# Performance work log

Measured on AMD Instinct MI355X. Metric: run time of the kernel, lower is better.

The kernel has to match this reference:

```python
import jax, jax.numpy as jnp
import numpy as np

D_MODEL = 1024
N_HEADS = 16
HEAD_DIM = D_MODEL // N_HEADS  # 64
WINDOW = 15
NUM_RANDOM = 2
B, L = 2, 2048


def setup_inputs() -> dict:
    key = jax.random.key(0)
    ks = jax.random.split(key, 5)
    x = jax.random.normal(ks[0], (B, L, D_MODEL), dtype=jnp.float32)
    # rotary angles: theta[t, j] = t / 10000^(2j/head_dim), shape [1, L, head_dim//2]
    inv_freq = 1.0 / (10000.0 ** (jnp.arange(0, HEAD_DIM, 2, dtype=jnp.float32) / HEAD_DIM))
    t = jnp.arange(L, dtype=jnp.float32)
    freqs = (t[:, None] * inv_freq[None, :])[None].astype(jnp.float32)  # [1,L,32]
    scale = 0.02
    wq = jax.random.normal(ks[1], (D_MODEL, D_MODEL), dtype=jnp.float32) * scale
    wk = jax.random.normal(ks[2], (D_MODEL, D_MODEL), dtype=jnp.float32) * scale
    wv = jax.random.normal(ks[3], (D_MODEL, D_MODEL), dtype=jnp.float32) * scale
    wo = jax.random.normal(ks[4], (D_MODEL, D_MODEL), dtype=jnp.float32) * scale
    return {"x": x, "freqs": freqs, "wq": wq, "wk": wk, "wv": wv, "wo": wo}


def _rope(t, cos, sin):
    # t: [B,H,L,hd]; interpret last dim as (hd/2, 2) complex pairs and rotate.
    tr = t.reshape(*t.shape[:-1], -1, 2)
    re, im = tr[..., 0], tr[..., 1]
    out_re = re * cos - im * sin
    out_im = re * sin + im * cos
    return jnp.stack([out_re, out_im], axis=-1).reshape(t.shape)


def _bigbird_mask(Lq):
    ii = jnp.arange(Lq)[:, None]
    jj = jnp.arange(Lq)[None, :]
    causal = jj <= ii
    window = jnp.abs(ii - jj) <= (WINDOW // 2)
    glob = (ii == 0) | (jj == 0)
    # random mask: per row i, NUM_RANDOM indices uniform in [0, i]
    rkey = jax.random.key(42)
    u = jax.random.uniform(rkey, (Lq, NUM_RANDOM))
    ridx = jnp.floor(u * (jnp.arange(Lq, dtype=jnp.float32)[:, None] + 1.0)).astype(jnp.int32)
    rmask = jnp.zeros((Lq, Lq), dtype=bool).at[jnp.arange(Lq)[:, None], ridx].set(True)
    # rows with <= NUM_RANDOM causal options attend to all of them
    rmask = rmask | (causal & (ii < NUM_RANDOM))
    return (causal & (window | rmask)) | glob  # [L,L]


def reference(x, freqs, wq, wk, wv, wo):
    b, l, _ = x.shape
    q = (x @ wq.T).reshape(b, l, N_HEADS, HEAD_DIM).transpose(0, 2, 1, 3)  # [B,H,L,hd]
    k = (x @ wk.T).reshape(b, l, N_HEADS, HEAD_DIM).transpose(0, 2, 1, 3)
    v = (x @ wv.T).reshape(b, l, N_HEADS, HEAD_DIM).transpose(0, 2, 1, 3)
    cos = jnp.cos(freqs[:, :l])[:, None]  # [1,1,L,hd/2]
    sin = jnp.sin(freqs[:, :l])[:, None]
    q = _rope(q, cos, sin)
    k = _rope(k, cos, sin)
    attn_mask = _bigbird_mask(l)  # [L,L], broadcast over B,H
    scale = 1.0 / jnp.sqrt(jnp.float32(HEAD_DIM))
    scores = jnp.einsum("bhqd,bhkd->bhqk", q, k) * scale
    scores = jnp.where(attn_mask[None, None], scores, jnp.finfo(scores.dtype).min)
    p = jax.nn.softmax(scores, axis=-1)
    out = jnp.einsum("bhqk,bhkd->bhqd", p, v)
    out = out.transpose(0, 2, 1, 3).reshape(b, l, D_MODEL)
    return out @ wo.T
```

## Files before the change

### kernel.cpp

```cpp
#include <hip/hip_runtime.h>
#include <math.h>

#define SEQ_L 2048
#define DM 1024
#define NH 16
#define HD 64
#define NB 2
#define KD 1024
#define ND 1024

typedef __bf16 bf16;
typedef __bf16 bf16x8 __attribute__((ext_vector_type(8)));
typedef __bf16 bf16x4 __attribute__((ext_vector_type(4)));
typedef __bf16 bf16x2 __attribute__((ext_vector_type(2)));
typedef float f32x4 __attribute__((ext_vector_type(4)));

__device__ inline uint32_t rotl32(uint32_t v, int n) { return (v << n) | (v >> (32 - n)); }

__device__ inline void threefry(uint32_t x0, uint32_t x1, uint32_t* o0, uint32_t* o1) {
  const uint32_t ks0 = 0u, ks1 = 42u, ks2 = 0u ^ 42u ^ 0x1BD11BDAu;
  x0 += ks0; x1 += ks1;
#define TF_R(rr) { x0 += x1; x1 = rotl32(x1, rr); x1 ^= x0; }
  TF_R(13) TF_R(15) TF_R(26) TF_R(6)
  x0 += ks1; x1 += ks2 + 1u;
  TF_R(17) TF_R(29) TF_R(16) TF_R(24)
  x0 += ks2; x1 += ks0 + 2u;
  TF_R(13) TF_R(15) TF_R(26) TF_R(6)
  x0 += ks0; x1 += ks1 + 3u;
  TF_R(17) TF_R(29) TF_R(16) TF_R(24)
  x0 += ks1; x1 += ks2 + 4u;
  TF_R(13) TF_R(15) TF_R(26) TF_R(6)
  x0 += ks2; x1 += ks0 + 5u;
#undef TF_R
  *o0 = x0; *o1 = x1;
}

__device__ inline int rand_col(int i, int s) {
  uint32_t o0, o1;
  threefry(0u, (uint32_t)(2 * i + s), &o0, &o1);
  uint32_t bits = o0 ^ o1;
  float u = __uint_as_float((bits >> 9) | 0x3f800000u) - 1.0f;
  return (int)floorf(u * (float)(i + 1));
}

__global__ void prep_kernel(const float* __restrict__ x,
                            const float* __restrict__ w0, const float* __restrict__ w1,
                            const float* __restrict__ w2, const float* __restrict__ w3,
                            const float* __restrict__ freqs,
                            bf16* __restrict__ xb,
                            bf16* __restrict__ o0, bf16* __restrict__ o1,
                            bf16* __restrict__ o2, bf16* __restrict__ o3,
                            int* __restrict__ ctab, float2* __restrict__ rtab) {
  const int bx = blockIdx.x;
  const int t = threadIdx.x;
  if (bx < 8192) {
    const float* src;
    bf16* dst;
    int idx;
    if (bx < 4096) { src = x; dst = xb; idx = bx * 256 + t; }
    else {
      int widx = bx - 4096;
      int wsel = widx >> 10;
      switch (wsel) {
        case 0: src = w0; dst = o0; break;
        case 1: src = w1; dst = o1; break;
        case 2: src = w2; dst = o2; break;
        default: src = w3; dst = o3; break;
      }
      idx = (widx & 1023) * 256 + t;
    }
    float4 vv = ((const float4*)src)[idx];
    bf16x4 ov;
    ov[0] = (bf16)vv.x; ov[1] = (bf16)vv.y; ov[2] = (bf16)vv.z; ov[3] = (bf16)vv.w;
    *(bf16x4*)(dst + (size_t)idx * 4) = ov;
    return;
  }
  if (bx < 8200) {
    const int i = (bx - 8192) * 256 + t;
    int cols[11]; int nc = 0;
    if (i >= 1) {
      int lo = i - 7; if (lo < 0) lo = 0;
      for (int j = lo; j <= i; ++j) cols[nc++] = j;
      if (lo > 0) cols[nc++] = 0;
#pragma unroll
      for (int s = 0; s < 2; ++s) {
        int rj = rand_col(i, s);
        bool dup = false;
        for (int c2 = 0; c2 < nc; ++c2) dup |= (cols[c2] == rj);
        if (!dup) cols[nc++] = rj;
      }
    }
    for (int c2 = nc; c2 < 11; ++c2) cols[c2] = -1;
#pragma unroll
    for (int c2 = 0; c2 < 11; ++c2) ctab[i * 12 + c2] = cols[c2];
    ctab[i * 12 + 11] = nc;
    return;
  }
  const int idx = (bx - 8200) * 256 + t;
  float s, c;
  sincosf(freqs[idx], &s, &c);
  rtab[idx] = make_float2(c, s);
}

__device__ inline void gld16(const bf16* g, bf16* l) {
  __builtin_amdgcn_global_load_lds((const __attribute__((address_space(1))) void*)g,
                                   (__attribute__((address_space(3))) void*)l, 16, 0, 0);
}

__global__ __launch_bounds__(256, 4) void qkv_gemm_kernel(
    const bf16* __restrict__ xb, const bf16* __restrict__ wqb, const bf16* __restrict__ wkb,
    const bf16* __restrict__ wvb, bf16* __restrict__ qb, bf16* __restrict__ kb, bf16* __restrict__ vb,
    const float2* __restrict__ rtab) {
  __shared__ __align__(16) bf16 As[64 * 64];
  __shared__ __align__(16) bf16 Bs[3][64 * 64];
  const bf16* Ws[3] = {wqb, wkb, wvb};
  bf16* Ds[3] = {qb, kb, vb};

  const int t = threadIdx.x;
  const int lane = t & 63;
  const int w = t >> 6;
  const int wm = (w >> 1) * 32;
  const int wn = (w & 1) * 32;
  const int m0 = blockIdx.x * 64;
  const int n0 = blockIdx.y * 64;
  const int l15 = lane & 15;
  const int kq = lane >> 4;

  f32x4 acc[3][2][2] = {};

  for (int k0 = 0; k0 < KD; k0 += 64) {
#pragma unroll
    for (int n = 0; n < 2; ++n) {
      const int s = n * 256 + t;
      const int row = s >> 3;
      const int ch = (s & 7) ^ (row & 7);
      gld16(xb + (size_t)(m0 + row) * KD + k0 + ch * 8, As + s * 8);
    }
#pragma unroll
    for (int j = 0; j < 3; ++j)
#pragma unroll
      for (int n = 0; n < 2; ++n) {
        const int s = n * 256 + t;
        const int row = s >> 3;
        const int ch = (s & 7) ^ (row & 7);
        gld16(Ws[j] + (size_t)(n0 + row) * KD + k0 + ch * 8, &Bs[j][s * 8]);
      }
    __syncthreads();
#pragma unroll
    for (int ks = 0; ks < 2; ++ks) {
      const int cb = ks * 4 + kq;
      bf16x8 af[2];
#pragma unroll
      for (int mt = 0; mt < 2; ++mt) {
        const int row = wm + mt * 16 + l15;
        af[mt] = *(const bf16x8*)(As + row * 64 + ((cb ^ (row & 7)) * 8));
      }
#pragma unroll
      for (int j = 0; j < 3; ++j) {
        bf16x8 bfr[2];
#pragma unroll
        for (int nt = 0; nt < 2; ++nt) {
          const int row = wn + nt * 16 + l15;
          bfr[nt] = *(const bf16x8*)(&Bs[j][row * 64 + ((cb ^ (row & 7)) * 8)]);
        }
#pragma unroll
        for (int mt = 0; mt < 2; ++mt)
#pragma unroll
          for (int nt = 0; nt < 2; ++nt)
            acc[j][mt][nt] = __builtin_amdgcn_mfma_f32_16x16x32_bf16(af[mt], bfr[nt], acc[j][mt][nt], 0, 0, 0);
      }
    }
    __syncthreads();
  }
  const int colb = n0 + wn + l15;
  const int rowb = m0 + wm + (lane >> 4) * 4;
  const int odd = l15 & 1;
#pragma unroll
  for (int j = 0; j < 3; ++j) {
    bf16* D = Ds[j];
    const bool dorope = (j < 2);
#pragma unroll
    for (int mt = 0; mt < 2; ++mt)
#pragma unroll
      for (int nt = 0; nt < 2; ++nt) {
        const int col = colb + nt * 16;
        const int jj = (col & 63) >> 1;
#pragma unroll
        for (int rr = 0; rr < 4; ++rr) {
          float val = acc[j][mt][nt][rr];
          float other = __shfl_xor(val, 1);
          if (!odd) {
            const int row = rowb + mt * 16 + rr;
            float lo, hi;
            if (dorope) {
              float2 cs = rtab[(row & (SEQ_L - 1)) * 32 + jj];
              lo = val * cs.x - other * cs.y;
              hi = val * cs.y + other * cs.x;
            } else { lo = val; hi = other; }
            bf16x2 p; p[0] = (bf16)lo; p[1] = (bf16)hi;
            *(bf16x2*)(D + (size_t)row * ND + col) = p;
          }
        }
      }
  }
}

__global__ __launch_bounds__(256, 2) void out_gemm_kernel(
    bf16* __restrict__ ab, const bf16* __restrict__ wob, float* __restrict__ out,
    const float* __restrict__ pm, const float* __restrict__ pz, const float* __restrict__ pv) {
  const int t = threadIdx.x;
  const int m0 = blockIdx.x * 64;
  const int n0 = blockIdx.y * 128;

  if (blockIdx.x == 0 || blockIdx.x == 32) {
    const int b = blockIdx.x == 0 ? 0 : 1;
#pragma unroll
    for (int e = t; e < DM; e += 256) {
      const int h = e >> 6, d = e & 63;
      const int base = b * 128 + h * 8;
      float M = -1e30f;
#pragma unroll
      for (int c = 0; c < 8; ++c) M = fmaxf(M, pm[base + c]);
      float Z = 0.f, od = 0.f;
#pragma unroll
      for (int c = 0; c < 8; ++c) {
        float sc = __expf(pm[base + c] - M);
        Z += pz[base + c] * sc;
        od += pv[(base + c) * 64 + d] * sc;
      }
      ab[(size_t)b * SEQ_L * DM + e] = (bf16)(od / Z);
    }
    __syncthreads();
  }

  __shared__ __align__(16) bf16 As[64 * 64];
  __shared__ __align__(16) bf16 Bs[128 * 64];
  const int lane = t & 63;
  const int wave = t >> 6;
  const int wm = (wave >> 1) * 32;
  const int wn = (wave & 1) * 64;
  const int l15 = lane & 15;
  const int kq = lane >> 4;

  f32x4 acc[2][4] = {};

  for (int k0 = 0; k0 < KD; k0 += 64) {
#pragma unroll
    for (int n = 0; n < 2; ++n) {
      const int s = n * 256 + t;
      const int row = s >> 3;
      const int ch = (s & 7) ^ (row & 7);
      gld16(ab + (size_t)(m0 + row) * KD + k0 + ch * 8, As + s * 8);
    }
#pragma unroll
    for (int n = 0; n < 4; ++n) {
      const int s = n * 256 + t;
      const int row = s >> 3;
      const int ch = (s & 7) ^ (row & 7);
      gld16(wob + (size_t)(n0 + row) * KD + k0 + ch * 8, Bs + s * 8);
    }
    __syncthreads();
#pragma unroll
    for (int ks = 0; ks < 2; ++ks) {
      const int cb = ks * 4 + kq;
      bf16x8 af[2], bfr[4];
#pragma unroll
      for (int mt = 0; mt < 2; ++mt) {
        const int row = wm + mt * 16 + l15;
        af[mt] = *(const bf16x8*)(As + row * 64 + ((cb ^ (row & 7)) * 8));
      }
#pragma unroll
      for (int nt = 0; nt < 4; ++nt) {
        const int row = wn + nt * 16 + l15;
        bfr[nt] = *(const bf16x8*)(Bs + row * 64 + ((cb ^ (row & 7)) * 8));
      }
#pragma unroll
      for (int mt = 0; mt < 2; ++mt)
#pragma unroll
        for (int nt = 0; nt < 4; ++nt)
          acc[mt][nt] = __builtin_amdgcn_mfma_f32_16x16x32_bf16(af[mt], bfr[nt], acc[mt][nt], 0, 0, 0);
    }
    __syncthreads();
  }
  const int colb = n0 + wn + l15;
  const int rowb = m0 + wm + (lane >> 4) * 4;
#pragma unroll
  for (int mt = 0; mt < 2; ++mt)
#pragma unroll
    for (int nt = 0; nt < 4; ++nt)
#pragma unroll
      for (int rr = 0; rr < 4; ++rr)
        out[(size_t)(rowb + mt * 16 + rr) * ND + colb + nt * 16] = acc[mt][nt][rr];
}

__global__ __launch_bounds__(256, 3) void attn_kernel(const bf16* __restrict__ q, const bf16* __restrict__ k,
                                                      const bf16* __restrict__ v, bf16* __restrict__ o,
                                                      const int* __restrict__ ctab,
                                                      float* __restrict__ pm, float* __restrict__ pz,
                                                      float* __restrict__ pv) {
  const int t = threadIdx.x;
  const int lane = t & 63;
  const int w = t >> 6;

  __shared__ float sbuf[256];
  __shared__ float redm[4], redz[4];
  __shared__ float part[4][64];

  if (blockIdx.x >= 256) {
    const int sbx = blockIdx.x - 256;
    const int b = sbx >> 9;
    const int tt = sbx & 511;
    const int tile = ((tt & 7) << 6) + (tt >> 3);
    const int i = tile * 4 + 1 + w;
    if (i >= SEQ_L) return;
    const size_t bb = (size_t)b * SEQ_L * DM;
    const int eo = lane * 16;

    const bf16* qrow = q + bb + (size_t)i * DM + eo;
    bf16x8 qv0 = *(const bf16x8*)(qrow);
    bf16x8 qv1 = *(const bf16x8*)(qrow + 8);

    const int4* cp = (const int4*)(ctab + i * 12);
    int4 ca = cp[0], cb = cp[1], cc = cp[2];
    int cols[11] = {ca.x, ca.y, ca.z, ca.w, cb.x, cb.y, cb.z, cb.w, cc.x, cc.y, cc.z};

    bf16x8 kv[11][2];
#pragma unroll
    for (int c = 0; c < 11; ++c) {
      int cj = cols[c] < 0 ? 0 : cols[c];
      const bf16* krow = k + bb + (size_t)cj * DM + eo;
      kv[c][0] = *(const bf16x8*)(krow);
      kv[c][1] = *(const bf16x8*)(krow + 8);
    }

    float sv[11];
#pragma unroll
    for (int c = 0; c < 11; ++c) {
      float acc = 0.f;
#pragma unroll
      for (int e = 0; e < 8; ++e)
        acc += (float)qv0[e] * (float)kv[c][0][e] + (float)qv1[e] * (float)kv[c][1][e];
      sv[c] = acc;
    }

    bf16x8 vv[11][2];
#pragma unroll
    for (int c = 0; c < 11; ++c) {
      int cj = cols[c] < 0 ? 0 : cols[c];
      const bf16* vrow = v + bb + (size_t)cj * DM + eo;
      vv[c][0] = *(const bf16x8*)(vrow);
      vv[c][1] = *(const bf16x8*)(vrow + 8);
    }

#pragma unroll
    for (int c = 0; c < 11; ++c) {
      sv[c] += __shfl_xor(sv[c], 1);
      sv[c] += __shfl_xor(sv[c], 2);
      sv[c] = cols[c] < 0 ? -1e30f : sv[c] * 0.125f;
    }
    float m = -1e30f;
#pragma unroll
    for (int c = 0; c < 11; ++c) m = fmaxf(m, sv[c]);
    float z = 0.f;
#pragma unroll
    for (int c = 0; c < 11; ++c) { sv[c] = __expf(sv[c] - m); z += sv[c]; }
    const float inv = 1.f / z;

    float oa[16] = {};
#pragma unroll
    for (int c = 0; c < 11; ++c) {
#pragma unroll
      for (int e = 0; e < 8; ++e) {
        oa[e]     += sv[c] * (float)vv[c][0][e];
        oa[8 + e] += sv[c] * (float)vv[c][1][e];
      }
    }
    bf16x8 ov0, ov1;
#pragma unroll
    for (int e = 0; e < 8; ++e) {
      ov0[e] = (bf16)(oa[e] * inv);
      ov1[e] = (bf16)(oa[8 + e] * inv);
    }
    bf16* orow = o + bb + (size_t)i * DM + eo;
    *(bf16x8*)(orow) = ov0;
    *(bf16x8*)(orow + 8) = ov1;
    return;
  }

  const int idx = blockIdx.x;
  const int b = idx >> 7;
  const int rem = idx & 127;
  const int h = rem >> 3;
  const int c = rem & 7;
  const size_t hb = (size_t)b * SEQ_L * DM + (size_t)h * HD;
  const int j = c * 256 + t;

  bf16x8 qv8[8];
#pragma unroll
  for (int cc = 0; cc < 8; ++cc) qv8[cc] = *(const bf16x8*)(q + hb + cc * 8);

  float acc = 0.f;
#pragma unroll
  for (int cc = 0; cc < 8; ++cc) {
    bf16x8 kv = *(const bf16x8*)(k + hb + (size_t)j * DM + cc * 8);
#pragma unroll
    for (int e = 0; e < 8; ++e) acc += (float)qv8[cc][e] * (float)kv[e];
  }
  float s = acc * 0.125f;
  float mloc = s;
#pragma unroll
  for (int off = 32; off > 0; off >>= 1) mloc = fmaxf(mloc, __shfl_xor(mloc, off));
  if (lane == 0) redm[w] = mloc;
  __syncthreads();
  const float m = fmaxf(fmaxf(redm[0], redm[1]), fmaxf(redm[2], redm[3]));

  float e = __expf(s - m);
  sbuf[t] = e;
  float zloc = e;
#pragma unroll
  for (int off = 32; off > 0; off >>= 1) zloc += __shfl_xor(zloc, off);
  if (lane == 0) redz[w] = zloc;
  __syncthreads();
  const float zc = redz[0] + redz[1] + redz[2] + redz[3];

  float oa = 0.f;
  for (int jj = w; jj < 256; jj += 4)
    oa += sbuf[jj] * (float)v[hb + (size_t)(c * 256 + jj) * DM + lane];
  part[w][lane] = oa;
  __syncthreads();
  if (t < 64) pv[idx * 64 + t] = part[0][t] + part[1][t] + part[2][t] + part[3][t];
  if (t == 0) { pm[idx] = m; pz[idx] = zc; }
}

extern "C" void kernel_launch(void* const* d_in, const int* in_sizes, int n_in,
                              void* d_out, int out_size, void* d_ws, size_t ws_size,
                              hipStream_t stream) {
  const float* x     = (const float*)d_in[0];
  const float* freqs = (const float*)d_in[1];
  const float* wq    = (const float*)d_in[2];
  const float* wk    = (const float*)d_in[3];
  const float* wv    = (const float*)d_in[4];
  const float* wo    = (const float*)d_in[5];
  float* out = (float*)d_out;

  char* ws = (char*)d_ws;
  bf16* xb  = (bf16*)(ws + 0);
  bf16* wqb = (bf16*)(ws + 8388608);
  bf16* wkb = (bf16*)(ws + 10485760);
  bf16* wvb = (bf16*)(ws + 12582912);
  bf16* wob = (bf16*)(ws + 14680064);
  bf16* qb  = (bf16*)(ws + 16777216);
  bf16* kb  = (bf16*)(ws + 25165824);
  bf16* vb  = (bf16*)(ws + 33554432);
  bf16* ab  = (bf16*)(ws + 41943040);
  int*    ctab = (int*)(ws + 50331648);
  float*  pm   = (float*)(ws + 50462720);
  float*  pz   = (float*)(ws + 50463744);
  float*  pv   = (float*)(ws + 50464768);
  float2* rtab = (float2*)(ws + 50593792);
  (void)ws_size;

  prep_kernel<<<8456, 256, 0, stream>>>(x, wq, wk, wv, wo, freqs, xb, wqb, wkb, wvb, wob, ctab, rtab);
  qkv_gemm_kernel<<<dim3(64, 16), 256, 0, stream>>>(xb, wqb, wkb, wvb, qb, kb, vb, rtab);
  attn_kernel<<<dim3(1280, 1), 256, 0, stream>>>(qb, kb, vb, ab, ctab, pm, pz, pv);
  out_gemm_kernel<<<dim3(64, 8), 256, 0, stream>>>(ab, wob, out, pm, pz, pv);
}
```

Before: 161.1 us.

## Double-buffer LDS tiles with BK=32 in QKV and output GEMMs

Both GEMM kernels (the fused QKV projection with RoPE and the output projection) now use two LDS buffers with a K-tile of 32 instead of a single 64-wide tile. The next tile's global-to-LDS loads are issued before computing on the current tile, so load latency overlaps with MFMA work. The XOR swizzle is adapted to the 32-wide rows and pointer offsets are precomputed. The trade-off is twice as many barriers per K, and each inner step does less MFMA work, which gives less to hide latency behind. The total LDS footprint is unchanged.

Result: slower. 169.6 us (+5.3%).

```diff
diff --git a/kernel.cpp b/kernel.cpp
--- a/kernel.cpp
+++ b/kernel.cpp
@@ -111,9 +111,8 @@
     const bf16* __restrict__ xb, const bf16* __restrict__ wqb, const bf16* __restrict__ wkb,
     const bf16* __restrict__ wvb, bf16* __restrict__ qb, bf16* __restrict__ kb, bf16* __restrict__ vb,
     const float2* __restrict__ rtab) {
-  __shared__ __align__(16) bf16 As[64 * 64];
-  __shared__ __align__(16) bf16 Bs[3][64 * 64];
-  const bf16* Ws[3] = {wqb, wkb, wvb};
+  __shared__ __align__(16) bf16 As0[64 * 32], As1[64 * 32];
+  __shared__ __align__(16) bf16 Bs0[3][64 * 32], Bs1[3][64 * 32];
   bf16* Ds[3] = {qb, kb, vb};
 
   const int t = threadIdx.x;
@@ -126,52 +125,60 @@
   const int l15 = lane & 15;
   const int kq = lane >> 4;
 
+  const int r0 = t >> 2;
+  const int chs = (t & 3) ^ ((r0 >> 1) & 3);
+  const size_t soff = (size_t)r0 * KD + chs * 8;
+  const bf16* pA  = xb  + (size_t)m0 * KD + soff;
+  const bf16* pB0 = wqb + (size_t)n0 * KD + soff;
+  const bf16* pB1 = wkb + (size_t)n0 * KD + soff;
+  const bf16* pB2 = wvb + (size_t)n0 * KD + soff;
+  const int t8 = t * 8;
+
   f32x4 acc[3][2][2] = {};
 
-  for (int k0 = 0; k0 < KD; k0 += 64) {
-#pragma unroll
-    for (int n = 0; n < 2; ++n) {
-      const int s = n * 256 + t;
-      const int row = s >> 3;
-      const int ch = (s & 7) ^ (row & 7);
-      gld16(xb + (size_t)(m0 + row) * KD + k0 + ch * 8, As + s * 8);
-    }
-#pragma unroll
-    for (int j = 0; j < 3; ++j)
-#pragma unroll
-      for (int n = 0; n < 2; ++n) {
-        const int s = n * 256 + t;
-        const int row = s >> 3;
-        const int ch = (s & 7) ^ (row & 7);
-        gld16(Ws[j] + (size_t)(n0 + row) * KD + k0 + ch * 8, &Bs[j][s * 8]);
-      }
+  auto stage = [&](int kt, bf16* A, bf16* B0, bf16* B1, bf16* B2) {
+    const int koff = kt * 32;
+    gld16(pA + koff, A + t8);
+    gld16(pB0 + koff, B0 + t8);
+    gld16(pB1 + koff, B1 + t8);
+    gld16(pB2 + koff, B2 + t8);
+  };
+  auto comp = [&](const bf16* A, const bf16* B0, const bf16* B1, const bf16* B2) {
+    bf16x8 af[2];
+#pragma unroll
+    for (int mt = 0; mt < 2; ++mt) {
+      const int row = wm + mt * 16 + l15;
+      af[mt] = *(const bf16x8*)(A + row * 32 + ((kq ^ ((row >> 1) & 3)) * 8));
+    }
+    const bf16* Bp[3] = {B0, B1, B2};
+#pragma unroll
+    for (int j = 0; j < 3; ++j) {
+      bf16x8 bfr[2];
+#pragma unroll
+      for (int nt = 0; nt < 2; ++nt) {
+        const int row = wn + nt * 16 + l15;
+        bfr[nt] = *(const bf16x8*)(Bp[j] + row * 32 + ((kq ^ ((row >> 1) & 3)) * 8));
+      }
+#pragma unroll
+      for (int mt = 0; mt < 2; ++mt)
+#pragma unroll
+        for (int nt = 0; nt < 2; ++nt)
+          acc[j][mt][nt] = __builtin_amdgcn_mfma_f32_16x16x32_bf16(af[mt], bfr[nt], acc[j][mt][nt], 0, 0, 0);
+    }
+  };
+
+  stage(0, As0, &Bs0[0][0], &Bs0[1][0], &Bs0[2][0]);
+  __syncthreads();
+
+  for (int kt = 0; kt < 32; kt += 2) {
+    stage(kt + 1, As1, &Bs1[0][0], &Bs1[1][0], &Bs1[2][0]);
+    comp(As0, &Bs0[0][0], &Bs0[1][0], &Bs0[2][0]);
     __syncthreads();
-#pragma unroll
-    for (int ks = 0; ks < 2; ++ks) {
-      const int cb = ks * 4 + kq;
-      bf16x8 af[2];
-#pragma unroll
-      for (int mt = 0; mt < 2; ++mt) {
-        const int row = wm + mt * 16 + l15;
-        af[mt] = *(const bf16x8*)(As + row * 64 + ((cb ^ (row & 7)) * 8));
-      }
-#pragma unroll
-      for (int j = 0; j < 3; ++j) {
-        bf16x8 bfr[2];
-#pragma unroll
-        for (int nt = 0; nt < 2; ++nt) {
-          const int row = wn + nt * 16 + l15;
-          bfr[nt] = *(const bf16x8*)(&Bs[j][row * 64 + ((cb ^ (row & 7)) * 8)]);
-        }
-#pragma unroll
-        for (int mt = 0; mt < 2; ++mt)
-#pragma unroll
-          for (int nt = 0; nt < 2; ++nt)
-            acc[j][mt][nt] = __builtin_amdgcn_mfma_f32_16x16x32_bf16(af[mt], bfr[nt], acc[j][mt][nt], 0, 0, 0);
-      }
-    }
+    if (kt + 2 < 32) stage(kt + 2, As0, &Bs0[0][0], &Bs0[1][0], &Bs0[2][0]);
+    comp(As1, &Bs1[0][0], &Bs1[1][0], &Bs1[2][0]);
     __syncthreads();
   }
+
   const int colb = n0 + wn + l15;
   const int rowb = m0 + wm + (lane >> 4) * 4;
   const int odd = l15 & 1;
@@ -233,8 +240,8 @@
     __syncthreads();
   }
 
-  __shared__ __align__(16) bf16 As[64 * 64];
-  __shared__ __align__(16) bf16 Bs[128 * 64];
+  __shared__ __align__(16) bf16 Ao0[64 * 32], Ao1[64 * 32];
+  __shared__ __align__(16) bf16 Bo0[128 * 32], Bo1[128 * 32];
   const int lane = t & 63;
   const int wave = t >> 6;
   const int wm = (wave >> 1) * 32;
@@ -242,46 +249,53 @@
   const int l15 = lane & 15;
   const int kq = lane >> 4;
 
+  const int r0 = t >> 2;
+  const int chs = (t & 3) ^ ((r0 >> 1) & 3);
+  const size_t soff = (size_t)r0 * KD + chs * 8;
+  const bf16* pA  = ab  + (size_t)m0 * KD + soff;
+  const bf16* pB0 = wob + (size_t)n0 * KD + soff;
+  const bf16* pB1 = pB0 + (size_t)64 * KD;
+  const int t8 = t * 8;
+
   f32x4 acc[2][4] = {};
 
-  for (int k0 = 0; k0 < KD; k0 += 64) {
-#pragma unroll
-    for (int n = 0; n < 2; ++n) {
-      const int s = n * 256 + t;
-      const int row = s >> 3;
-      const int ch = (s & 7) ^ (row & 7);
-      gld16(ab + (size_t)(m0 + row) * KD + k0 + ch * 8, As + s * 8);
-    }
-#pragma unroll
-    for (int n = 0; n < 4; ++n) {
-      const int s = n * 256 + t;
-      const int row = s >> 3;
-      const int ch = (s & 7) ^ (row & 7);
-      gld16(wob + (size_t)(n0 + row) * KD + k0 + ch * 8, Bs + s * 8);
-    }
+  auto stage = [&](int kt, bf16* A, bf16* B) {
+    const int koff = kt * 32;
+    gld16(pA + koff, A + t8);
+    gld16(pB0 + koff, B + t8);
+    gld16(pB1 + koff, B + 2048 + t8);
+  };
+  auto comp = [&](const bf16* A, const bf16* B) {
+    bf16x8 af[2], bfr[4];
+#pragma unroll
+    for (int mt = 0; mt < 2; ++mt) {
+      const int row = wm + mt * 16 + l15;
+      af[mt] = *(const bf16x8*)(A + row * 32 + ((kq ^ ((row >> 1) & 3)) * 8));
+    }
+#pragma unroll
+    for (int nt = 0; nt < 4; ++nt) {
+      const int row = wn + nt * 16 + l15;
+      bfr[nt] = *(const bf16x8*)(B + row * 32 + ((kq ^ ((row >> 1) & 3)) * 8));
+    }
+#pragma unroll
+    for (int mt = 0; mt < 2; ++mt)
+#pragma unroll
+      for (int nt = 0; nt < 4; ++nt)
+        acc[mt][nt] = __builtin_amdgcn_mfma_f32_16x16x32_bf16(af[mt], bfr[nt], acc[mt][nt], 0, 0, 0);
+  };
+
+  stage(0, Ao0, Bo0);
+  __syncthreads();
+
+  for (int kt = 0; kt < 32; kt += 2) {
+    stage(kt + 1, Ao1, Bo1);
+    comp(Ao0, Bo0);
     __syncthreads();
-#pragma unroll
-    for (int ks = 0; ks < 2; ++ks) {
-      const int cb = ks * 4 + kq;
-      bf16x8 af[2], bfr[4];
-#pragma unroll
-      for (int mt = 0; mt < 2; ++mt) {
-        const int row = wm + mt * 16 + l15;
-        af[mt] = *(const bf16x8*)(As + row * 64 + ((cb ^ (row & 7)) * 8));
-      }
-#pragma unroll
-      for (int nt = 0; nt < 4; ++nt) {
-        const int row = wn + nt * 16 + l15;
-        bfr[nt] = *(const bf16x8*)(Bs + row * 64 + ((cb ^ (row & 7)) * 8));
-      }
-#pragma unroll
-      for (int mt = 0; mt < 2; ++mt)
-#pragma unroll
-        for (int nt = 0; nt < 4; ++nt)
-          acc[mt][nt] = __builtin_amdgcn_mfma_f32_16x16x32_bf16(af[mt], bfr[nt], acc[mt][nt], 0, 0, 0);
-    }
+    if (kt + 2 < 32) stage(kt + 2, Ao0, Bo0);
+    comp(Ao1, Bo1);
     __syncthreads();
   }
+
   const int colb = n0 + wn + l15;
   const int rowb = m0 + wm + (lane >> 4) * 4;
 #pragma unroll
```
